# Optimization experiments

Measured on AMD Instinct MI355X. Metric: run time of the kernel, lower is better.

## Reference

```python
import jax, jax.numpy as jnp
import numpy as np

K_CONST = 1.0  # margin constant K from __init__


def setup_inputs() -> dict:
    key = jax.random.key(0)
    k1, k2, k3 = jax.random.split(key, 3)
    m, n, d = 2048, 100000, 128
    return {
        "X_tilde": jax.random.normal(k1, (m, d), dtype=jnp.float32),
        "X": jax.random.normal(k2, (n, d), dtype=jnp.float32),
        "w": jax.random.normal(k3, (n, 1), dtype=jnp.float32),
        "k": 10,
    }


def reference(X_tilde, X, w, k):
    # w_prime = sqrt((max(w) - w) / K), appended as extra coordinate for the
    # augmented exact L2 search (queries padded with 0 in that coordinate).
    w_prime2 = (jnp.max(w) - w)[:, 0] / K_CONST  # (n,) == w_prime**2
    # squared L2 in augmented space: ||q||^2 + ||x||^2 + w_prime^2 - 2 q.x
    q2 = jnp.sum(X_tilde * X_tilde, axis=1, keepdims=True)           # (m,1)
    x2 = jnp.sum(X * X, axis=1) + w_prime2                            # (n,)
    d2 = q2 + x2[None, :] - 2.0 * (X_tilde @ X.T)                     # (m,n)
    _, idx = jax.lax.top_k(-d2, k)                                    # (m,k) nearest
    # gather neighbors and recompute actual (non-augmented) L2 distance
    nb = X[idx]                                                       # (m,k,d)
    diff = nb - X_tilde[:, None, :]
    dist = jnp.sqrt(jnp.sum(diff * diff, axis=2))                     # (m,k)
    act = w[idx, 0] - K_CONST * dist                                  # (m,k)
    # argmax + gather == max over the k neighbors
    return jnp.max(act, axis=1)                                       # (m,)
```

## Files before the change

kernel.cpp:

```cpp
#include <hip/hip_runtime.h>
#include <math.h>

typedef __attribute__((ext_vector_type(8))) short short8;
typedef __attribute__((ext_vector_type(16))) float f32x16;

#define D      128
#define NSEG   128
#define SEGC   800
#define NT     25
#define TILE_C 32
#define KTOP   10
#define CAP    128
#define DELTA  3.0f
#define NPAD   (NSEG * SEGC + TILE_C)
#define ROWU   144
#define TUNITS (TILE_C * 18)
#define BUFU   (TUNITS * 8)

__device__ __forceinline__ int lds_unit(int u) {
    int r = u / 18, kb = u % 18;
    return r * 18 + (kb ^ ((r >> 2) & 1));
}

__device__ __forceinline__ ushort f2bf(float f) {
    uint u = __float_as_uint(f);
    uint r = (u + 0x7FFFu + ((u >> 16) & 1u)) >> 16;
    return (ushort)r;
}

__device__ __forceinline__ uint packx2(float x2w) {
    ushort h = f2bf(x2w);
    float hf = __uint_as_float(((uint)h) << 16);
    ushort lo = f2bf(x2w - hf);
    return (uint)h | ((uint)lo << 16);
}

__device__ __forceinline__ void insert10(float s, float v, float ls[KTOP], float lw[KTOP]) {
    ls[9] = s; lw[9] = v;
#pragma unroll
    for (int p = 9; p > 0; --p) {
        bool sw = ls[p] < ls[p - 1];
        float ts = sw ? ls[p - 1] : ls[p];
        float tl = sw ? ls[p]     : ls[p - 1];
        float tv = sw ? lw[p - 1] : lw[p];
        float tu = sw ? lw[p]     : lw[p - 1];
        ls[p] = ts; ls[p - 1] = tl;
        lw[p] = tv; lw[p - 1] = tu;
    }
}

__device__ __forceinline__ void insert10s(float s, float ms[KTOP]) {
    ms[9] = s;
#pragma unroll
    for (int p = 9; p > 0; --p) {
        float a = fminf(ms[p - 1], ms[p]);
        float b = fmaxf(ms[p - 1], ms[p]);
        ms[p - 1] = a; ms[p] = b;
    }
}

__global__ void prep_kernel(const float* __restrict__ Xt, const float* __restrict__ X,
                            const float* __restrict__ w,
                            ushort* __restrict__ Xbp, ushort* __restrict__ Xtb,
                            float* __restrict__ x2wf, float* __restrict__ q2f,
                            int* __restrict__ cnt, int n, int m, int nblocksA) {
    int wave = threadIdx.x >> 6, lane = threadIdx.x & 63;
    if ((int)blockIdx.x < nblocksA) {
        int row = blockIdx.x * 4 + wave;
        if (row >= NPAD) return;
        ushort* rowp = Xbp + (size_t)row * ROWU;
        if (row < n) {
            float2 v = ((const float2*)X)[(size_t)row * 64 + lane];
            ((ushort2*)rowp)[lane] = make_ushort2(f2bf(v.x), f2bf(v.y));
            float s = v.x * v.x + v.y * v.y;
#pragma unroll
            for (int o = 32; o; o >>= 1) s += __shfl_xor(s, o, 64);
            float x2w = s - w[row];
            if (lane == 0) x2wf[row] = x2w;
            if (lane < 8) ((uint*)rowp)[64 + lane] = (lane == 0) ? packx2(x2w) : 0u;
        } else {
            ((ushort2*)rowp)[lane] = make_ushort2(0, 0);
            if (lane < 8) ((uint*)rowp)[64 + lane] = (lane == 0) ? packx2(1e30f) : 0u;
        }
    } else {
        int qb = blockIdx.x - nblocksA;
        int row = qb * 4 + wave;
        int tid = qb * 256 + threadIdx.x;
        if (tid < m) cnt[tid] = 0;
        if (row >= m) return;
        float2 v = ((const float2*)Xt)[(size_t)row * 64 + lane];
        ((ushort2*)Xtb)[(size_t)row * 64 + lane] = make_ushort2(f2bf(v.x), f2bf(v.y));
        float s = v.x * v.x + v.y * v.y;
#pragma unroll
        for (int o = 32; o; o >>= 1) s += __shfl_xor(s, o, 64);
        if (lane == 0) q2f[row] = s;
    }
}

__device__ __forceinline__ void emit_cand(int q, int c, int* cnt, int* buf) {
    int pos = atomicAdd(&cnt[q], 1);
    if (pos < CAP) buf[q * CAP + pos] = c;
}

template<int PASS>
__global__ __launch_bounds__(256, 4) void nd_pass(
        const ushort* __restrict__ Xbp, const ushort* __restrict__ Xtb,
        const float* __restrict__ tau, float* __restrict__ minbuf,
        int* __restrict__ cnt, int* __restrict__ buf, int m) {
    __shared__ __align__(16) ushort As[2 * BUFU];

    const int t = threadIdx.x;
    const int l = t & 63, wv = t >> 6;
    const int half = l >> 5;
    const int seg = blockIdx.x;
    const int qbase = blockIdx.y * 256 + wv * 64;
    const int q0 = qbase + (l & 31);
    const int tile0 = seg * NT;
    const int halfx = half ^ ((l >> 2) & 1);

    short8 Bf[8][2];
#pragma unroll
    for (int s = 0; s < 8; ++s)
#pragma unroll
        for (int qs = 0; qs < 2; ++qs)
            Bf[s][qs] = *(const short8*)(Xtb + (size_t)(q0 + qs * 32) * D + s * 16 + half * 8);
    short8 B8 = (short8)(short)0;
    if (l < 32) { B8[0] = (short)0xBF00; B8[1] = (short)0xBF00; }

    float tp[2];
    float mx[2];
#pragma unroll
    for (int qs = 0; qs < 2; ++qs) {
        tp[qs] = (PASS == 2) ? (-0.5f * tau[q0 + qs * 32]) : 0.f;
        mx[qs] = -INFINITY;
    }

    const int u0 = t, u1 = 256 + t, u2 = 512 + (t & 63);
    const int L0 = lds_unit(u0) * 8, L1 = lds_unit(u1) * 8, L2 = lds_unit(u2) * 8;
    const uint4* Xg = (const uint4*)Xbp;

    uint4 r0 = Xg[(size_t)tile0 * TUNITS + u0];
    uint4 r1 = Xg[(size_t)tile0 * TUNITS + u1];
    uint4 r2 = make_uint4(0, 0, 0, 0);
    if (t < 64) r2 = Xg[(size_t)tile0 * TUNITS + u2];

    for (int t2 = 0; t2 < NT; ++t2) {
        ushort* Lb = &As[(t2 & 1) * BUFU];
        *(uint4*)&Lb[L0] = r0;
        *(uint4*)&Lb[L1] = r1;
        if (t < 64) *(uint4*)&Lb[L2] = r2;
        __syncthreads();

        const size_t gb = (size_t)(tile0 + t2 + 1) * TUNITS;
        r0 = Xg[gb + u0];
        r1 = Xg[gb + u1];
        if (t < 64) r2 = Xg[gb + u2];

        f32x16 acc0 = (f32x16)0.f, acc1 = (f32x16)0.f;
#pragma unroll
        for (int ks = 0; ks < 9; ++ks) {
            const int kb = (ks < 8) ? (ks * 2 + halfx) : (16 + halfx);
            short8 a = *(const short8*)&Lb[((l & 31) * 18 + kb) * 8];
            short8 b0 = (ks < 8) ? Bf[ks][0] : B8;
            short8 b1 = (ks < 8) ? Bf[ks][1] : B8;
            acc0 = __builtin_amdgcn_mfma_f32_32x32x16_bf16(a, b0, acc0, 0, 0, 0);
            acc1 = __builtin_amdgcn_mfma_f32_32x32x16_bf16(a, b1, acc1, 0, 0, 0);
        }

        float h[2];
        h[0] = -INFINITY; h[1] = -INFINITY;
#pragma unroll
        for (int r = 0; r < 16; ++r) {
            h[0] = fmaxf(h[0], acc0[r]); h[1] = fmaxf(h[1], acc1[r]);
        }
        if (PASS == 1) {
            mx[0] = fmaxf(mx[0], h[0]);
            mx[1] = fmaxf(mx[1], h[1]);
        } else {
            const int base = (tile0 + t2) * TILE_C;
            if (__any(h[0] >= tp[0])) {
#pragma unroll
                for (int r = 0; r < 16; ++r)
                    if (acc0[r] >= tp[0]) emit_cand(q0,      base + (r & 3) + 8 * (r >> 2) + 4 * half, cnt, buf);
            }
            if (__any(h[1] >= tp[1])) {
#pragma unroll
                for (int r = 0; r < 16; ++r)
                    if (acc1[r] >= tp[1]) emit_cand(q0 + 32, base + (r & 3) + 8 * (r >> 2) + 4 * half, cnt, buf);
            }
        }
    }

    if (PASS == 1) {
        size_t rowi = (size_t)(seg * 2 + half) * m;
        minbuf[rowi + q0]      = -2.f * mx[0];
        minbuf[rowi + q0 + 32] = -2.f * mx[1];
    }
}

__global__ void tau_kernel(const float* __restrict__ minbuf, float* __restrict__ tau, int m) {
    __shared__ float sh[64 * 40];
    const int qi = threadIdx.x & 63, part = threadIdx.x >> 6;
    const int q = blockIdx.x * 64 + qi;
    float ms[KTOP];
#pragma unroll
    for (int e = 0; e < KTOP; ++e) ms[e] = INFINITY;
#pragma unroll 4
    for (int i = 0; i < 64; ++i) {
        float v = minbuf[(size_t)(part * 64 + i) * m + q];
        if (v < ms[9]) insert10s(v, ms);
    }
#pragma unroll
    for (int e = 0; e < KTOP; ++e) sh[qi * 40 + part * 10 + e] = ms[e];
    __syncthreads();
    if (threadIdx.x < 64) {
        const int qq = blockIdx.x * 64 + threadIdx.x;
        float fs[KTOP];
#pragma unroll
        for (int e = 0; e < KTOP; ++e) fs[e] = INFINITY;
        for (int x = 0; x < 40; ++x) {
            float v = sh[threadIdx.x * 40 + x];
            if (v < fs[9]) insert10s(v, fs);
        }
        tau[qq] = fs[9] + DELTA;
    }
}

__global__ void rescore_kernel(const float* __restrict__ Xtf, const float* __restrict__ Xf,
                               const float* __restrict__ w, const float* __restrict__ x2wf,
                               const float* __restrict__ q2f, const int* __restrict__ cnt,
                               const int* __restrict__ buf, float* __restrict__ out, int m) {
    __shared__ float sS[CAP], sW[CAP];
    const int q = blockIdx.x, l = threadIdx.x;
    const int c = min(cnt[q], CAP);
    const bool v0 = l < c, v1 = l + 64 < c;
    const int j0 = v0 ? buf[q * CAP + l] : 0;
    const int j1 = v1 ? buf[q * CAP + l + 64] : 0;
    const float4* Q4 = (const float4*)Xtf + (size_t)q * 32;
    const float4* A4 = (const float4*)Xf + (size_t)j0 * 32;
    const float4* B4 = (const float4*)Xf + (size_t)j1 * 32;
    float acc0 = 0.f, acc1 = 0.f;
#pragma unroll 8
    for (int d = 0; d < 32; ++d) {
        float4 qv = Q4[d];
        float4 a = A4[d], b = B4[d];
        acc0 = fmaf(qv.x, a.x, fmaf(qv.y, a.y, fmaf(qv.z, a.z, fmaf(qv.w, a.w, acc0))));
        acc1 = fmaf(qv.x, b.x, fmaf(qv.y, b.y, fmaf(qv.z, b.z, fmaf(qv.w, b.w, acc1))));
    }
    sS[l]      = v0 ? (x2wf[j0] - 2.f * acc0) : INFINITY;
    sW[l]      = v0 ? w[j0] : 0.f;
    sS[l + 64] = v1 ? (x2wf[j1] - 2.f * acc1) : INFINITY;
    sW[l + 64] = v1 ? w[j1] : 0.f;
    __syncthreads();
    if (l == 0) {
        float ls[KTOP], lw[KTOP];
#pragma unroll
        for (int e = 0; e < KTOP; ++e) { ls[e] = INFINITY; lw[e] = 0.f; }
        for (int i = 0; i < c; ++i)
            if (sS[i] < ls[9]) insert10(sS[i], sW[i], ls, lw);
        float q2v = q2f[q];
        float mxv = -INFINITY;
#pragma unroll
        for (int e = 0; e < KTOP; ++e) {
            if (ls[e] < 1e30f) {
                float d2 = fmaxf(q2v + ls[e] + lw[e], 0.f);
                mxv = fmaxf(mxv, lw[e] - sqrtf(d2));
            }
        }
        out[q] = mxv;
    }
}

extern "C" void kernel_launch(void* const* d_in, const int* in_sizes, int n_in,
                              void* d_out, int out_size, void* d_ws, size_t ws_size,
                              hipStream_t stream) {
    const float* Xt = (const float*)d_in[0];
    const float* X  = (const float*)d_in[1];
    const float* w  = (const float*)d_in[2];
    const int m = in_sizes[0] / D;
    const int n = in_sizes[1] / D;

    auto align256 = [](size_t x) { return (x + 255) & ~(size_t)255; };
    char* p = (char*)d_ws;
    ushort* Xbp  = (ushort*)p;  p += align256((size_t)NPAD * ROWU * 2);
    ushort* Xtb  = (ushort*)p;  p += align256((size_t)m * D * 2);
    float*  x2wf = (float*)p;   p += align256((size_t)n * 4);
    float*  q2f  = (float*)p;   p += align256((size_t)m * 4);
    float*  minb = (float*)p;   p += align256((size_t)2 * NSEG * m * 4);
    float*  tau  = (float*)p;   p += align256((size_t)m * 4);
    int*    cnt  = (int*)p;     p += align256((size_t)m * 4);
    int*    buf  = (int*)p;     p += align256((size_t)m * CAP * 4);

    const int nblocksA = (NPAD + 3) / 4;
    const int nblocksB = (m + 3) / 4;
    prep_kernel<<<nblocksA + nblocksB, 256, 0, stream>>>(Xt, X, w, Xbp, Xtb, x2wf, q2f, cnt, n, m, nblocksA);

    dim3 grid(NSEG, m / 256);
    nd_pass<1><<<grid, 256, 0, stream>>>(Xbp, Xtb, tau, minb, cnt, buf, m);
    tau_kernel<<<m / 64, 256, 0, stream>>>(minb, tau, m);
    nd_pass<2><<<grid, 256, 0, stream>>>(Xbp, Xtb, tau, minb, cnt, buf, m);
    rescore_kernel<<<m, 64, 0, stream>>>(Xt, X, w, x2wf, q2f, cnt, buf, (float*)d_out, m);
}
```

Measured before the change: 273.1 us.

## Prune pass-2 to segments whose pass-1 minimum is within the threshold

Pass 2 no longer rescans every (segment, query) pair. A new list_build kernel compacts, per segment, the queries whose segment minimum from pass 1 falls under tau, then enqueues work items split into 5-tile parts. A persistent nd_pass2 grid then processes only those items. This is meant to skip most of the MFMA and tile loading in pass 2, at the cost of an extra kernel, indirect query loads, per-item B-fragment reloads and a work-queue atomic.

```diff
diff --git a/kernel.cpp b/kernel.cpp
--- a/kernel.cpp
+++ b/kernel.cpp
@@ -8,6 +8,8 @@
 #define NSEG   128
 #define SEGC   800
 #define NT     25
+#define TPP    5
+#define NPART  5
 #define TILE_C 32
 #define KTOP   10
 #define CAP    128
@@ -16,6 +18,8 @@
 #define ROWU   144
 #define TUNITS (TILE_C * 18)
 #define BUFU   (TUNITS * 8)
+#define MQ     2048
+#define WQCAP  (NSEG * 8 * NPART)
 
 __device__ __forceinline__ int lds_unit(int u) {
     int r = u / 18, kb = u % 18;
@@ -63,7 +67,9 @@
                             const float* __restrict__ w,
                             ushort* __restrict__ Xbp, ushort* __restrict__ Xtb,
                             float* __restrict__ x2wf, float* __restrict__ q2f,
-                            int* __restrict__ cnt, int n, int m, int nblocksA) {
+                            int* __restrict__ cnt, int* __restrict__ wq_n,
+                            int n, int m, int nblocksA) {
+    if (blockIdx.x == 0 && threadIdx.x == 0) wq_n[0] = 0;
     int wave = threadIdx.x >> 6, lane = threadIdx.x & 63;
     if ((int)blockIdx.x < nblocksA) {
         int row = blockIdx.x * 4 + wave;
@@ -102,11 +108,9 @@
     if (pos < CAP) buf[q * CAP + pos] = c;
 }
 
-template<int PASS>
-__global__ __launch_bounds__(256, 4) void nd_pass(
+__global__ __launch_bounds__(256, 4) void nd_pass1(
         const ushort* __restrict__ Xbp, const ushort* __restrict__ Xtb,
-        const float* __restrict__ tau, float* __restrict__ minbuf,
-        int* __restrict__ cnt, int* __restrict__ buf, int m) {
+        float* __restrict__ minbuf, int m) {
     __shared__ __align__(16) ushort As[2 * BUFU];
 
     const int t = threadIdx.x;
@@ -127,13 +131,7 @@
     short8 B8 = (short8)(short)0;
     if (l < 32) { B8[0] = (short)0xBF00; B8[1] = (short)0xBF00; }
 
-    float tp[2];
-    float mx[2];
-#pragma unroll
-    for (int qs = 0; qs < 2; ++qs) {
-        tp[qs] = (PASS == 2) ? (-0.5f * tau[q0 + qs * 32]) : 0.f;
-        mx[qs] = -INFINITY;
-    }
+    float mx0 = -INFINITY, mx1 = -INFINITY;
 
     const int u0 = t, u1 = 256 + t, u2 = 512 + (t & 63);
     const int L0 = lds_unit(u0) * 8, L1 = lds_unit(u1) * 8, L2 = lds_unit(u2) * 8;
@@ -167,35 +165,16 @@
             acc1 = __builtin_amdgcn_mfma_f32_32x32x16_bf16(a, b1, acc1, 0, 0, 0);
         }
 
-        float h[2];
-        h[0] = -INFINITY; h[1] = -INFINITY;
-#pragma unroll
-        for (int r = 0; r < 16; ++r) {
-            h[0] = fmaxf(h[0], acc0[r]); h[1] = fmaxf(h[1], acc1[r]);
-        }
-        if (PASS == 1) {
-            mx[0] = fmaxf(mx[0], h[0]);
-            mx[1] = fmaxf(mx[1], h[1]);
-        } else {
-            const int base = (tile0 + t2) * TILE_C;
-            if (__any(h[0] >= tp[0])) {
-#pragma unroll
-                for (int r = 0; r < 16; ++r)
-                    if (acc0[r] >= tp[0]) emit_cand(q0,      base + (r & 3) + 8 * (r >> 2) + 4 * half, cnt, buf);
-            }
-            if (__any(h[1] >= tp[1])) {
-#pragma unroll
-                for (int r = 0; r < 16; ++r)
-                    if (acc1[r] >= tp[1]) emit_cand(q0 + 32, base + (r & 3) + 8 * (r >> 2) + 4 * half, cnt, buf);
-            }
-        }
-    }
-
-    if (PASS == 1) {
-        size_t rowi = (size_t)(seg * 2 + half) * m;
-        minbuf[rowi + q0]      = -2.f * mx[0];
-        minbuf[rowi + q0 + 32] = -2.f * mx[1];
-    }
+        float h0 = -INFINITY, h1 = -INFINITY;
+#pragma unroll
+        for (int r = 0; r < 16; ++r) { h0 = fmaxf(h0, acc0[r]); h1 = fmaxf(h1, acc1[r]); }
+        mx0 = fmaxf(mx0, h0);
+        mx1 = fmaxf(mx1, h1);
+    }
+
+    size_t rowi = (size_t)(seg * 2 + half) * m;
+    minbuf[rowi + q0]      = -2.f * mx0;
+    minbuf[rowi + q0 + 32] = -2.f * mx1;
 }
 
 __global__ void tau_kernel(const float* __restrict__ minbuf, float* __restrict__ tau, int m) {
@@ -223,6 +202,118 @@
             if (v < fs[9]) insert10s(v, fs);
         }
         tau[qq] = fs[9] + DELTA;
+    }
+}
+
+__global__ void list_build(const float* __restrict__ minbuf, const float* __restrict__ tau,
+                           int* __restrict__ qlist, int* __restrict__ wq,
+                           int* __restrict__ wq_n, int m) {
+    __shared__ int lq[MQ];
+    __shared__ int lcnt;
+    const int s = blockIdx.x, tid = threadIdx.x;
+    if (tid == 0) lcnt = 0;
+    __syncthreads();
+    const float* r0 = minbuf + (size_t)(2 * s) * m;
+    const float* r1 = minbuf + (size_t)(2 * s + 1) * m;
+    for (int q = tid; q < m; q += 256) {
+        float v = fminf(r0[q], r1[q]);
+        if (v <= tau[q]) { int p = atomicAdd(&lcnt, 1); lq[p] = q; }
+    }
+    __syncthreads();
+    const int c = lcnt;
+    const int padded = (c + 255) & ~255;
+    for (int i = c + tid; i < padded; i += 256) lq[i] = -1;
+    __syncthreads();
+    for (int i = tid; i < padded; i += 256) qlist[(size_t)s * MQ + i] = lq[i];
+    if (tid == 0 && c > 0) {
+        const int nqc = padded >> 8;
+        int base = atomicAdd(wq_n, nqc * NPART);
+        for (int qc = 0; qc < nqc; ++qc)
+            for (int p = 0; p < NPART; ++p)
+                wq[base++] = (s << 6) | (qc << 3) | p;
+    }
+}
+
+__global__ __launch_bounds__(256, 4) void nd_pass2(
+        const ushort* __restrict__ Xbp, const ushort* __restrict__ Xtb,
+        const float* __restrict__ tau,
+        int* __restrict__ cnt, int* __restrict__ buf,
+        const int* __restrict__ qlist, const int* __restrict__ wq,
+        const int* __restrict__ wq_n, int m) {
+    __shared__ __align__(16) ushort As[2 * BUFU];
+
+    const int t = threadIdx.x;
+    const int l = t & 63, wv = t >> 6;
+    const int half = l >> 5;
+    const int halfx = half ^ ((l >> 2) & 1);
+    const int u0 = t, u1 = 256 + t, u2 = 512 + (t & 63);
+    const int L0 = lds_unit(u0) * 8, L1 = lds_unit(u1) * 8, L2 = lds_unit(u2) * 8;
+    const uint4* Xg = (const uint4*)Xbp;
+    const int T = wq_n[0];
+
+    for (int w = blockIdx.x; w < T; w += gridDim.x) {
+        const int it = wq[w];
+        const int s = it >> 6, qc = (it >> 3) & 7, part = it & 7;
+        const int t0 = s * NT + part * TPP;
+        const int lbase = s * MQ + qc * 256 + wv * 64 + (l & 31);
+        const int qi0 = qlist[lbase], qi1 = qlist[lbase + 32];
+        const int q0e = qi0 < 0 ? 0 : qi0, q1e = qi1 < 0 ? 0 : qi1;
+
+        short8 Bf[8][2];
+#pragma unroll
+        for (int sk = 0; sk < 8; ++sk) {
+            Bf[sk][0] = *(const short8*)(Xtb + (size_t)q0e * D + sk * 16 + half * 8);
+            Bf[sk][1] = *(const short8*)(Xtb + (size_t)q1e * D + sk * 16 + half * 8);
+        }
+        short8 B8 = (short8)(short)0;
+        if (l < 32) { B8[0] = (short)0xBF00; B8[1] = (short)0xBF00; }
+        const float tp0 = (qi0 < 0) ? INFINITY : (-0.5f * tau[qi0]);
+        const float tp1 = (qi1 < 0) ? INFINITY : (-0.5f * tau[qi1]);
+
+        uint4 r0 = Xg[(size_t)t0 * TUNITS + u0];
+        uint4 r1 = Xg[(size_t)t0 * TUNITS + u1];
+        uint4 r2 = make_uint4(0, 0, 0, 0);
+        if (t < 64) r2 = Xg[(size_t)t0 * TUNITS + u2];
+
+        for (int t2 = t0; t2 < t0 + TPP; ++t2) {
+            ushort* Lb = &As[(t2 & 1) * BUFU];
+            *(uint4*)&Lb[L0] = r0;
+            *(uint4*)&Lb[L1] = r1;
+            if (t < 64) *(uint4*)&Lb[L2] = r2;
+            __syncthreads();
+
+            const size_t gb = (size_t)(t2 + 1) * TUNITS;
+            r0 = Xg[gb + u0];
+            r1 = Xg[gb + u1];
+            if (t < 64) r2 = Xg[gb + u2];
+
+            f32x16 acc0 = (f32x16)0.f, acc1 = (f32x16)0.f;
+#pragma unroll
+            for (int ks = 0; ks < 9; ++ks) {
+                const int kb = (ks < 8) ? (ks * 2 + halfx) : (16 + halfx);
+                short8 a = *(const short8*)&Lb[((l & 31) * 18 + kb) * 8];
+                short8 b0 = (ks < 8) ? Bf[ks][0] : B8;
+                short8 b1 = (ks < 8) ? Bf[ks][1] : B8;
+                acc0 = __builtin_amdgcn_mfma_f32_32x32x16_bf16(a, b0, acc0, 0, 0, 0);
+                acc1 = __builtin_amdgcn_mfma_f32_32x32x16_bf16(a, b1, acc1, 0, 0, 0);
+            }
+
+            float h0 = -INFINITY, h1 = -INFINITY;
+#pragma unroll
+            for (int r = 0; r < 16; ++r) { h0 = fmaxf(h0, acc0[r]); h1 = fmaxf(h1, acc1[r]); }
+            const int base = t2 * TILE_C;
+            if (__any(h0 >= tp0)) {
+#pragma unroll
+                for (int r = 0; r < 16; ++r)
+                    if (acc0[r] >= tp0) emit_cand(qi0, base + (r & 3) + 8 * (r >> 2) + 4 * half, cnt, buf);
+            }
+            if (__any(h1 >= tp1)) {
+#pragma unroll
+                for (int r = 0; r < 16; ++r)
+                    if (acc1[r] >= tp1) emit_cand(qi1, base + (r & 3) + 8 * (r >> 2) + 4 * half, cnt, buf);
+            }
+        }
+        __syncthreads();
     }
 }
 
@@ -290,14 +381,19 @@
     float*  tau  = (float*)p;   p += align256((size_t)m * 4);
     int*    cnt  = (int*)p;     p += align256((size_t)m * 4);
     int*    buf  = (int*)p;     p += align256((size_t)m * CAP * 4);
+    int*    qlist= (int*)p;     p += align256((size_t)NSEG * MQ * 4);
+    int*    wq   = (int*)p;     p += align256((size_t)WQCAP * 4);
+    int*    wq_n = (int*)p;     p += align256((size_t)256);
 
     const int nblocksA = (NPAD + 3) / 4;
     const int nblocksB = (m + 3) / 4;
-    prep_kernel<<<nblocksA + nblocksB, 256, 0, stream>>>(Xt, X, w, Xbp, Xtb, x2wf, q2f, cnt, n, m, nblocksA);
-
-    dim3 grid(NSEG, m / 256);
-    nd_pass<1><<<grid, 256, 0, stream>>>(Xbp, Xtb, tau, minb, cnt, buf, m);
+    prep_kernel<<<nblocksA + nblocksB, 256, 0, stream>>>(Xt, X, w, Xbp, Xtb, x2wf, q2f,
+                                                         cnt, wq_n, n, m, nblocksA);
+
+    dim3 grid1(NSEG, m / 256);
+    nd_pass1<<<grid1, 256, 0, stream>>>(Xbp, Xtb, minb, m);
     tau_kernel<<<m / 64, 256, 0, stream>>>(minb, tau, m);
-    nd_pass<2><<<grid, 256, 0, stream>>>(Xbp, Xtb, tau, minb, cnt, buf, m);
+    list_build<<<NSEG, 256, 0, stream>>>(minb, tau, qlist, wq, wq_n, m);
+    nd_pass2<<<1024, 256, 0, stream>>>(Xbp, Xtb, tau, cnt, buf, qlist, wq, wq_n, m);
     rescore_kernel<<<m, 64, 0, stream>>>(Xt, X, w, x2wf, q2f, cnt, buf, (float*)d_out, m);
 }
```

After: 251.6 us (median of 2 runs). 7.9% less time.
